# Kernel optimization log

Hardware: AMD Instinct MI355X
Metric: run time of the kernel (lower is better)

Reference implementation:

```python
import jax, jax.numpy as jnp
import numpy as np

SCALE_POS = 2.0
SCALE_NEG = 40.0
THRESH_POS = 0.5
THRESH_NEG = 0.5
MARGIN = 0.1
EPS = 1e-5


def setup_inputs() -> dict:
    key = jax.random.key(0)
    kf, kl = jax.random.split(key)
    B, D, NUM_CLASSES = 4096, 1024, 64
    feats = jax.random.normal(kf, (B, D), dtype=jnp.float32)
    feats = feats / jnp.linalg.norm(feats, axis=1, keepdims=True)  # L2-normalized embeddings
    labels = jax.random.randint(kl, (B,), 0, NUM_CLASSES, dtype=jnp.int64)
    return {"feats": feats, "labels": labels}


def reference(feats, labels):
    B = feats.shape[0]
    sim = jnp.matmul(feats, feats.T)  # [B, B]
    same = labels[:, None] == labels[None, :]
    pos_mask = same & (sim < 1.0 - EPS)  # drop self / near-duplicate pairs
    neg_mask = ~same

    # hard mining: keep negatives above min positive - margin, positives below max negative + margin
    min_pos = jnp.min(jnp.where(pos_mask, sim, jnp.inf), axis=1)   # [B]
    max_neg = jnp.max(jnp.where(neg_mask, sim, -jnp.inf), axis=1)  # [B]
    neg_sel = neg_mask & (sim + MARGIN > min_pos[:, None])
    pos_sel = pos_mask & (sim - MARGIN < max_neg[:, None])

    pos_sum = jnp.sum(jnp.where(pos_sel, jnp.exp(-SCALE_POS * (sim - THRESH_POS)), 0.0), axis=1)
    neg_sum = jnp.sum(jnp.where(neg_sel, jnp.exp(SCALE_NEG * (sim - THRESH_NEG)), 0.0), axis=1)
    pos_loss = jnp.log1p(pos_sum) / SCALE_POS
    neg_loss = jnp.log1p(neg_sum) / SCALE_NEG

    valid = jnp.any(pos_sel, axis=1) & jnp.any(neg_sel, axis=1)  # rows skipped by original loop
    return jnp.sum(jnp.where(valid, pos_loss + neg_loss, 0.0)) / B
```

## Files before the change

kernel.cpp:

```cpp
#include <hip/hip_runtime.h>

typedef short short8 __attribute__((ext_vector_type(8)));
typedef _Float16 half8 __attribute__((ext_vector_type(8)));
typedef float floatx4 __attribute__((ext_vector_type(4)));
typedef __attribute__((address_space(1))) const void gvoid;
typedef __attribute__((address_space(3))) void svoid;

#define SCALE_POS 2.0f
#define SCALE_NEG 40.0f
#define THRESH 0.5f
#define MARGIN 0.1f
#define EPSV 1e-5f

__device__ __forceinline__ unsigned short f2bf(float f) {
    unsigned u = __float_as_uint(f);
    u += 0x7fffu + ((u >> 16) & 1u);
    return (unsigned short)(u >> 16);
}
__device__ __forceinline__ unsigned f2ord(float f) {
    unsigned u = __float_as_uint(f);
    return (u & 0x80000000u) ? ~u : (u | 0x80000000u);
}
__device__ __forceinline__ float ord2f(unsigned e) {
    unsigned v = (e & 0x80000000u) ? (e & 0x7fffffffu) : ~e;
    return __uint_as_float(v);
}

#define ORD_POS_INF 0xff800000u
#define ORD_NEG_INF 0x007fffffu

__global__ void k_init(const float* __restrict__ feats,
                       unsigned short* __restrict__ fb16,
                       unsigned* __restrict__ minp, unsigned* __restrict__ maxn,
                       float* __restrict__ psum, float* __restrict__ nsum,
                       int total4, int B) {
    int i = blockIdx.x * blockDim.x + threadIdx.x;
    if (i < total4) {
        float4 v = ((const float4*)feats)[i];
        ushort4 o;
        o.x = f2bf(v.x); o.y = f2bf(v.y); o.z = f2bf(v.z); o.w = f2bf(v.w);
        ((ushort4*)fb16)[i] = o;
    }
    if (i < B) {
        minp[i] = ORD_POS_INF;
        maxn[i] = ORD_NEG_INF;
        psum[i] = 0.f;
        nsum[i] = 0.f;
    }
}

__global__ void k_gemm_sym(const unsigned short* __restrict__ fb16,
                           const int* __restrict__ labels,
                           unsigned* __restrict__ minp_ord,
                           unsigned* __restrict__ maxn_ord,
                           _Float16* __restrict__ simh,
                           int D, int nb) {
    __shared__ __align__(16) unsigned short As[128 * 32];
    __shared__ __align__(16) unsigned short Bs[128 * 32];
    __shared__ int labR[128], labC[128];

    int t = blockIdx.x;
    int rb = 0, rem = t;
    while (rem >= nb - rb) { rem -= nb - rb; ++rb; }
    const int cb = rb + rem;

    const int tid = threadIdx.x;
    const int lane = tid & 63;
    const int wave = tid >> 6;
    const int wr = wave >> 1, wc = wave & 1;
    const int rowBase = rb * 128;
    const int colBase = cb * 128;

    if (tid < 128) labR[tid] = labels[rowBase + tid];
    else           labC[tid - 128] = labels[colBase + tid - 128];

    const int c0 = wave * 2, c1 = wave * 2 + 1;
    const int srow = lane >> 2;
    const int scol = (lane & 3) * 8;
    const unsigned short* gA0 = fb16 + (size_t)(rowBase + c0 * 16 + srow) * D + scol;
    const unsigned short* gA1 = fb16 + (size_t)(rowBase + c1 * 16 + srow) * D + scol;
    const unsigned short* gB0 = fb16 + (size_t)(colBase + c0 * 16 + srow) * D + scol;
    const unsigned short* gB1 = fb16 + (size_t)(colBase + c1 * 16 + srow) * D + scol;
    unsigned short* lA0 = As + c0 * 512 + lane * 8;
    unsigned short* lA1 = As + c1 * 512 + lane * 8;
    unsigned short* lB0 = Bs + c0 * 512 + lane * 8;
    unsigned short* lB1 = Bs + c1 * 512 + lane * 8;

    const int q = lane >> 4;
    const int cIn = lane & 15;
    int aOff[4], bOff[4];
#pragma unroll
    for (int i = 0; i < 4; ++i) {
        aOff[i] = (wr * 64 + i * 16 + cIn) * 32 + q * 8;
        bOff[i] = (wc * 64 + i * 16 + cIn) * 32 + q * 8;
    }

    floatx4 acc[4][4] = {};

    const int KT = D >> 5;
    for (int kt = 0; kt < KT; ++kt) {
        const int kOff = kt * 32;
        __syncthreads();
        __builtin_amdgcn_global_load_lds((gvoid*)(gA0 + kOff), (svoid*)lA0, 16, 0, 0);
        __builtin_amdgcn_global_load_lds((gvoid*)(gA1 + kOff), (svoid*)lA1, 16, 0, 0);
        __builtin_amdgcn_global_load_lds((gvoid*)(gB0 + kOff), (svoid*)lB0, 16, 0, 0);
        __builtin_amdgcn_global_load_lds((gvoid*)(gB1 + kOff), (svoid*)lB1, 16, 0, 0);
        __syncthreads();

        short8 a[4], b[4];
#pragma unroll
        for (int i = 0; i < 4; ++i) a[i] = *(const short8*)(As + aOff[i]);
#pragma unroll
        for (int i = 0; i < 4; ++i) b[i] = *(const short8*)(Bs + bOff[i]);
#pragma unroll
        for (int i = 0; i < 4; ++i)
#pragma unroll
            for (int j = 0; j < 4; ++j)
                acc[i][j] = __builtin_amdgcn_mfma_f32_16x16x32_bf16(a[i], b[j], acc[i][j], 0, 0, 0);
    }

    int rLabv[16];
#pragma unroll
    for (int mi = 0; mi < 4; ++mi)
#pragma unroll
        for (int rr = 0; rr < 4; ++rr)
            rLabv[mi * 4 + rr] = labR[wr * 64 + mi * 16 + q * 4 + rr];
    int cLabv[4];
#pragma unroll
    for (int ni = 0; ni < 4; ++ni)
        cLabv[ni] = labC[wc * 64 + ni * 16 + cIn];

    {
        half8* dst = (half8*)(simh + (size_t)t * 16384 + (size_t)tid * 64);
#pragma unroll
        for (int mi = 0; mi < 4; ++mi) {
            half8 h0, h1;
#pragma unroll
            for (int ni = 0; ni < 2; ++ni)
#pragma unroll
                for (int rr = 0; rr < 4; ++rr) {
                    h0[ni * 4 + rr] = (_Float16)acc[mi][ni][rr];
                    h1[ni * 4 + rr] = (_Float16)acc[mi][ni + 2][rr];
                }
            dst[mi * 2] = h0;
            dst[mi * 2 + 1] = h1;
        }
    }

#pragma unroll
    for (int mi = 0; mi < 4; ++mi) {
#pragma unroll
        for (int rr = 0; rr < 4; ++rr) {
            const int rLoc = wr * 64 + mi * 16 + q * 4 + rr;
            const int rLab = rLabv[mi * 4 + rr];
            float vmin = 1e30f, vmax = -1e30f;
#pragma unroll
            for (int ni = 0; ni < 4; ++ni) {
                float s = acc[mi][ni][rr];
                if (rLab == cLabv[ni]) {
                    if (s < 1.0f - EPSV) vmin = fminf(vmin, s);
                } else {
                    vmax = fmaxf(vmax, s);
                }
            }
#pragma unroll
            for (int off = 8; off; off >>= 1) {
                vmin = fminf(vmin, __shfl_xor(vmin, off, 16));
                vmax = fmaxf(vmax, __shfl_xor(vmax, off, 16));
            }
            if (cIn == 0) {
                if (vmin < 1e30f) atomicMin(&minp_ord[rowBase + rLoc], f2ord(vmin));
                if (vmax > -1e30f) atomicMax(&maxn_ord[rowBase + rLoc], f2ord(vmax));
            }
        }
    }

    if (rb != cb) {
#pragma unroll
        for (int ni = 0; ni < 4; ++ni) {
            const int cLab = cLabv[ni];
            float vmin = 1e30f, vmax = -1e30f;
#pragma unroll
            for (int mi = 0; mi < 4; ++mi)
#pragma unroll
                for (int rr = 0; rr < 4; ++rr) {
                    float s = acc[mi][ni][rr];
                    if (rLabv[mi * 4 + rr] == cLab) {
                        if (s < 1.0f - EPSV) vmin = fminf(vmin, s);
                    } else {
                        vmax = fmaxf(vmax, s);
                    }
                }
            vmin = fminf(vmin, __shfl_xor(vmin, 16, 64));
            vmin = fminf(vmin, __shfl_xor(vmin, 32, 64));
            vmax = fmaxf(vmax, __shfl_xor(vmax, 16, 64));
            vmax = fmaxf(vmax, __shfl_xor(vmax, 32, 64));
            if (q == 0) {
                const int cLoc = wc * 64 + ni * 16 + cIn;
                if (vmin < 1e30f) atomicMin(&minp_ord[colBase + cLoc], f2ord(vmin));
                if (vmax > -1e30f) atomicMax(&maxn_ord[colBase + cLoc], f2ord(vmax));
            }
        }
    }
}

__global__ void k_sum2(const _Float16* __restrict__ simh,
                       const int* __restrict__ labels,
                       const unsigned* __restrict__ minp_ord,
                       const unsigned* __restrict__ maxn_ord,
                       float* __restrict__ psum, float* __restrict__ nsum,
                       int nb) {
    __shared__ int labR[128], labC[128];
    __shared__ float mpR[128], mnR[128], mpC[128], mnC[128];

    int t = blockIdx.x;
    int rb = 0, rem = t;
    while (rem >= nb - rb) { rem -= nb - rb; ++rb; }
    const int cb = rb + rem;

    const int tid = threadIdx.x;
    const int lane = tid & 63;
    const int wave = tid >> 6;
    const int wr = wave >> 1, wc = wave & 1;
    const int rowBase = rb * 128;
    const int colBase = cb * 128;
    const int q = lane >> 4;
    const int cIn = lane & 15;

    if (tid < 128) {
        labR[tid] = labels[rowBase + tid];
        mpR[tid] = ord2f(minp_ord[rowBase + tid]);
        mnR[tid] = ord2f(maxn_ord[rowBase + tid]);
    } else {
        int j = tid - 128;
        labC[j] = labels[colBase + j];
        mpC[j] = ord2f(minp_ord[colBase + j]);
        mnC[j] = ord2f(maxn_ord[colBase + j]);
    }
    __syncthreads();

    int rLabv[16];
    float mpRv[16], mnRv[16];
#pragma unroll
    for (int mi = 0; mi < 4; ++mi)
#pragma unroll
        for (int rr = 0; rr < 4; ++rr) {
            int rLoc = wr * 64 + mi * 16 + q * 4 + rr;
            rLabv[mi * 4 + rr] = labR[rLoc];
            mpRv[mi * 4 + rr] = mpR[rLoc] - MARGIN;
            mnRv[mi * 4 + rr] = mnR[rLoc] + MARGIN;
        }
    int cLabv[4];
    float mpCv[4], mnCv[4];
#pragma unroll
    for (int ni = 0; ni < 4; ++ni) {
        int cLoc = wc * 64 + ni * 16 + cIn;
        cLabv[ni] = labC[cLoc];
        mpCv[ni] = mpC[cLoc] - MARGIN;
        mnCv[ni] = mnC[cLoc] + MARGIN;
    }

    const half8* src = (const half8*)(simh + (size_t)t * 16384 + (size_t)tid * 64);
    half8 hv[8];
#pragma unroll
    for (int v = 0; v < 8; ++v) hv[v] = src[v];

    float rps[16] = {}, rns[16] = {};
    float cps[4] = {}, cns[4] = {};
    const bool offd = (rb != cb);

#pragma unroll
    for (int mi = 0; mi < 4; ++mi)
#pragma unroll
        for (int ni = 0; ni < 4; ++ni)
#pragma unroll
            for (int rr = 0; rr < 4; ++rr) {
                const int idx = mi * 16 + ni * 4 + rr;
                const float s = (float)hv[idx >> 3][idx & 7];
                const int ri = mi * 4 + rr;
                if (rLabv[ri] == cLabv[ni]) {
                    if (s < 1.0f - EPSV) {
                        float e = __expf(-SCALE_POS * (s - THRESH));
                        if (s < mnRv[ri]) rps[ri] += e;
                        if (offd && s < mnCv[ni]) cps[ni] += e;
                    }
                } else {
                    float e = __expf(SCALE_NEG * (s - THRESH));
                    if (s > mpRv[ri]) rns[ri] += e;
                    if (offd && s > mpCv[ni]) cns[ni] += e;
                }
            }

#pragma unroll
    for (int i = 0; i < 16; ++i) {
#pragma unroll
        for (int off = 8; off; off >>= 1) {
            rps[i] += __shfl_xor(rps[i], off, 16);
            rns[i] += __shfl_xor(rns[i], off, 16);
        }
        if (cIn == 0) {
            const int rLoc = wr * 64 + (i >> 2) * 16 + q * 4 + (i & 3);
            if (rps[i] != 0.f) atomicAdd(&psum[rowBase + rLoc], rps[i]);
            if (rns[i] != 0.f) atomicAdd(&nsum[rowBase + rLoc], rns[i]);
        }
    }
    if (offd) {
#pragma unroll
        for (int ni = 0; ni < 4; ++ni) {
            cps[ni] += __shfl_xor(cps[ni], 16, 64);
            cps[ni] += __shfl_xor(cps[ni], 32, 64);
            cns[ni] += __shfl_xor(cns[ni], 16, 64);
            cns[ni] += __shfl_xor(cns[ni], 32, 64);
            if (q == 0) {
                const int cLoc = wc * 64 + ni * 16 + cIn;
                if (cps[ni] != 0.f) atomicAdd(&psum[colBase + cLoc], cps[ni]);
                if (cns[ni] != 0.f) atomicAdd(&nsum[colBase + cLoc], cns[ni]);
            }
        }
    }
}

template <int PASS>
__global__ void k_gemm(const unsigned short* __restrict__ fb16,
                       const int* __restrict__ labels,
                       unsigned* __restrict__ minp_ord,
                       unsigned* __restrict__ maxn_ord,
                       float* __restrict__ psum,
                       float* __restrict__ nsum,
                       int D) {
    __shared__ __align__(16) unsigned short As[128 * 32];
    __shared__ __align__(16) unsigned short Bs[128 * 32];
    __shared__ int labR[128], labC[128];
    __shared__ float mpS[128], mnS[128];

    const int tid = threadIdx.x;
    const int lane = tid & 63;
    const int wave = tid >> 6;
    const int wr = wave >> 1, wc = wave & 1;
    const int rowBase = blockIdx.y * 128;
    const int colBase = blockIdx.x * 128;

    if (tid < 128) {
        labR[tid] = labels[rowBase + tid];
        if (PASS == 2) {
            mpS[tid] = ord2f(minp_ord[rowBase + tid]);
            mnS[tid] = ord2f(maxn_ord[rowBase + tid]);
        }
    } else {
        labC[tid - 128] = labels[colBase + tid - 128];
    }

    const int c0 = wave * 2, c1 = wave * 2 + 1;
    const int srow = lane >> 2;
    const int scol = (lane & 3) * 8;
    const unsigned short* gA0 = fb16 + (size_t)(rowBase + c0 * 16 + srow) * D + scol;
    const unsigned short* gA1 = fb16 + (size_t)(rowBase + c1 * 16 + srow) * D + scol;
    const unsigned short* gB0 = fb16 + (size_t)(colBase + c0 * 16 + srow) * D + scol;
    const unsigned short* gB1 = fb16 + (size_t)(colBase + c1 * 16 + srow) * D + scol;
    unsigned short* lA0 = As + c0 * 512 + lane * 8;
    unsigned short* lA1 = As + c1 * 512 + lane * 8;
    unsigned short* lB0 = Bs + c0 * 512 + lane * 8;
    unsigned short* lB1 = Bs + c1 * 512 + lane * 8;

    const int q = lane >> 4;
    const int cIn = lane & 15;
    int aOff[4], bOff[4];
#pragma unroll
    for (int i = 0; i < 4; ++i) {
        aOff[i] = (wr * 64 + i * 16 + cIn) * 32 + q * 8;
        bOff[i] = (wc * 64 + i * 16 + cIn) * 32 + q * 8;
    }

    floatx4 acc[4][4] = {};

    const int KT = D >> 5;
    for (int kt = 0; kt < KT; ++kt) {
        const int kOff = kt * 32;
        __syncthreads();
        __builtin_amdgcn_global_load_lds((gvoid*)(gA0 + kOff), (svoid*)lA0, 16, 0, 0);
        __builtin_amdgcn_global_load_lds((gvoid*)(gA1 + kOff), (svoid*)lA1, 16, 0, 0);
        __builtin_amdgcn_global_load_lds((gvoid*)(gB0 + kOff), (svoid*)lB0, 16, 0, 0);
        __builtin_amdgcn_global_load_lds((gvoid*)(gB1 + kOff), (svoid*)lB1, 16, 0, 0);
        __syncthreads();

        short8 a[4], b[4];
#pragma unroll
        for (int i = 0; i < 4; ++i) a[i] = *(const short8*)(As + aOff[i]);
#pragma unroll
        for (int i = 0; i < 4; ++i) b[i] = *(const short8*)(Bs + bOff[i]);
#pragma unroll
        for (int i = 0; i < 4; ++i)
#pragma unroll
            for (int j = 0; j < 4; ++j)
                acc[i][j] = __builtin_amdgcn_mfma_f32_16x16x32_bf16(a[i], b[j], acc[i][j], 0, 0, 0);
    }

#pragma unroll
    for (int mi = 0; mi < 4; ++mi) {
#pragma unroll
        for (int r = 0; r < 4; ++r) {
            const int rLoc = wr * 64 + mi * 16 + q * 4 + r;
            const int rLab = labR[rLoc];
            if (PASS == 1) {
                float vmin = 1e30f, vmax = -1e30f;
#pragma unroll
                for (int ni = 0; ni < 4; ++ni) {
                    float s = acc[mi][ni][r];
                    int cLab = labC[wc * 64 + ni * 16 + cIn];
                    if (rLab == cLab) {
                        if (s < 1.0f - EPSV) vmin = fminf(vmin, s);
                    } else {
                        vmax = fmaxf(vmax, s);
                    }
                }
#pragma unroll
                for (int off = 8; off; off >>= 1) {
                    vmin = fminf(vmin, __shfl_xor(vmin, off, 16));
                    vmax = fmaxf(vmax, __shfl_xor(vmax, off, 16));
                }
                if (cIn == 0) {
                    if (vmin < 1e30f) atomicMin(&minp_ord[rowBase + rLoc], f2ord(vmin));
                    if (vmax > -1e30f) atomicMax(&maxn_ord[rowBase + rLoc], f2ord(vmax));
                }
            } else {
                const float mp = mpS[rLoc] - MARGIN;
                const float mn = mnS[rLoc] + MARGIN;
                float ps = 0.f, ns = 0.f;
#pragma unroll
                for (int ni = 0; ni < 4; ++ni) {
                    float s = acc[mi][ni][r];
                    int cLab = labC[wc * 64 + ni * 16 + cIn];
                    if (rLab == cLab) {
                        if (s < 1.0f - EPSV && s < mn) ps += expf(-SCALE_POS * (s - THRESH));
                    } else {
                        if (s > mp) ns += expf(SCALE_NEG * (s - THRESH));
                    }
                }
#pragma unroll
                for (int off = 8; off; off >>= 1) {
                    ps += __shfl_xor(ps, off, 16);
                    ns += __shfl_xor(ns, off, 16);
                }
                if (cIn == 0) {
                    if (ps != 0.f) atomicAdd(&psum[rowBase + rLoc], ps);
                    if (ns != 0.f) atomicAdd(&nsum[rowBase + rLoc], ns);
                }
            }
        }
    }
}

__global__ void k_final(const float* __restrict__ psum, const float* __restrict__ nsum,
                        float* __restrict__ out, int B) {
    __shared__ float red[4];
    float acc = 0.f;
    for (int i = threadIdx.x; i < B; i += 256) {
        float p = psum[i], n = nsum[i];
        if (p > 0.f && n > 0.f)
            acc += log1pf(p) * (1.0f / SCALE_POS) + log1pf(n) * (1.0f / SCALE_NEG);
    }
#pragma unroll
    for (int off = 32; off; off >>= 1) acc += __shfl_down(acc, off, 64);
    if ((threadIdx.x & 63) == 0) red[threadIdx.x >> 6] = acc;
    __syncthreads();
    if (threadIdx.x == 0) out[0] = (red[0] + red[1] + red[2] + red[3]) / (float)B;
}

extern "C" void kernel_launch(void* const* d_in, const int* in_sizes, int n_in,
                              void* d_out, int out_size, void* d_ws, size_t ws_size,
                              hipStream_t stream) {
    const float* feats = (const float*)d_in[0];
    const int* labels = (const int*)d_in[1];
    const int B = in_sizes[1];
    const int D = in_sizes[0] / B;
    const int nb = B / 128;
    const int NT = nb * (nb + 1) / 2;

    char* ws = (char*)d_ws;
    unsigned short* fb16 = (unsigned short*)ws;
    size_t off = (size_t)B * D * sizeof(unsigned short);
    unsigned* minp = (unsigned*)(ws + off); off += (size_t)B * 4;
    unsigned* maxn = (unsigned*)(ws + off); off += (size_t)B * 4;
    float* psum = (float*)(ws + off); off += (size_t)B * 4;
    float* nsum = (float*)(ws + off); off += (size_t)B * 4;
    _Float16* simh = (_Float16*)(ws + ((off + 255) & ~(size_t)255));
    size_t need = ((off + 255) & ~(size_t)255) + (size_t)NT * 16384 * sizeof(_Float16);

    const int total4 = B * D / 4;
    k_init<<<(total4 + 255) / 256, 256, 0, stream>>>(feats, fb16, minp, maxn, psum, nsum, total4, B);

    if (ws_size >= need) {
        k_gemm_sym<<<NT, 256, 0, stream>>>(fb16, labels, minp, maxn, simh, D, nb);
        k_sum2<<<NT, 256, 0, stream>>>(simh, labels, minp, maxn, psum, nsum, nb);
    } else {
        dim3 grid(B / 128, B / 128);
        k_gemm<1><<<grid, 256, 0, stream>>>(fb16, labels, minp, maxn, psum, nsum, D);
        k_gemm<2><<<grid, 256, 0, stream>>>(fb16, labels, minp, maxn, psum, nsum, D);
    }

    k_final<<<1, 256, 0, stream>>>(psum, nsum, (float*)d_out, B);
}
```

Before: 165.6 us.

## Fuse init, symmetric GEMM, mining and loss into one cooperative kernel

Replaces the multi-kernel pipeline (init, symmetric GEMM writing fp16 similarity tiles, sum pass, final reduction) with one cooperative kernel. It keeps each tile's accumulators in registers across grid.sync barriers, so the fp16 similarity matrix is never written or reread and several launches go away. With B=4096 the grid is 528 blocks, and cooperative launch needs them all resident, so it depends on the launch-bounds occupancy of 3 blocks per CU. If the launch fails it falls back to the old path. The fallback's non-symmetric branch now launches k_gemm_sym even when the workspace is too small for the simh buffer, and k_sum2's per-row registers were restructured.

```diff
diff --git a/kernel.cpp b/kernel.cpp
--- a/kernel.cpp
+++ b/kernel.cpp
@@ -1,4 +1,7 @@
 #include <hip/hip_runtime.h>
+#include <hip/hip_cooperative_groups.h>
+
+namespace cg = cooperative_groups;
 
 typedef short short8 __attribute__((ext_vector_type(8)));
 typedef _Float16 half8 __attribute__((ext_vector_type(8)));
@@ -28,6 +31,243 @@
 
 #define ORD_POS_INF 0xff800000u
 #define ORD_NEG_INF 0x007fffffu
+
+__global__ void __launch_bounds__(256, 3)
+k_fused(const float* __restrict__ feats, const int* __restrict__ labels,
+        unsigned short* __restrict__ fb16,
+        unsigned* __restrict__ minp_ord, unsigned* __restrict__ maxn_ord,
+        float* __restrict__ psum, float* __restrict__ nsum,
+        float* __restrict__ out,
+        int D, int nb, int B, int total4) {
+    cg::grid_group grid = cg::this_grid();
+
+    __shared__ __align__(16) unsigned short As[128 * 32];
+    __shared__ __align__(16) unsigned short Bs[128 * 32];
+    __shared__ int labR[128], labC[128];
+    __shared__ float mpR[128], mnR[128], mpC[128], mnC[128];
+    __shared__ float red[4];
+
+    const int tid = threadIdx.x;
+
+    {
+        const int gtid = blockIdx.x * 256 + tid;
+        const int gsz = gridDim.x * 256;
+        for (int i = gtid; i < total4; i += gsz) {
+            float4 v = ((const float4*)feats)[i];
+            ushort4 o;
+            o.x = f2bf(v.x); o.y = f2bf(v.y); o.z = f2bf(v.z); o.w = f2bf(v.w);
+            ((ushort4*)fb16)[i] = o;
+        }
+        for (int i = gtid; i < B; i += gsz) {
+            minp_ord[i] = ORD_POS_INF;
+            maxn_ord[i] = ORD_NEG_INF;
+            psum[i] = 0.f;
+            nsum[i] = 0.f;
+        }
+    }
+
+    int t = blockIdx.x;
+    int rb = 0, rem = t;
+    while (rem >= nb - rb) { rem -= nb - rb; ++rb; }
+    const int cb = rb + rem;
+
+    const int lane = tid & 63;
+    const int wave = tid >> 6;
+    const int wr = wave >> 1, wc = wave & 1;
+    const int rowBase = rb * 128;
+    const int colBase = cb * 128;
+    const int q = lane >> 4;
+    const int cIn = lane & 15;
+
+    if (tid < 128) labR[tid] = labels[rowBase + tid];
+    else           labC[tid - 128] = labels[colBase + tid - 128];
+
+    grid.sync();
+
+    const int c0 = wave * 2, c1 = wave * 2 + 1;
+    const int srow = lane >> 2;
+    const int scol = (lane & 3) * 8;
+    const unsigned short* gA0 = fb16 + (size_t)(rowBase + c0 * 16 + srow) * D + scol;
+    const unsigned short* gA1 = fb16 + (size_t)(rowBase + c1 * 16 + srow) * D + scol;
+    const unsigned short* gB0 = fb16 + (size_t)(colBase + c0 * 16 + srow) * D + scol;
+    const unsigned short* gB1 = fb16 + (size_t)(colBase + c1 * 16 + srow) * D + scol;
+    unsigned short* lA0 = As + c0 * 512 + lane * 8;
+    unsigned short* lA1 = As + c1 * 512 + lane * 8;
+    unsigned short* lB0 = Bs + c0 * 512 + lane * 8;
+    unsigned short* lB1 = Bs + c1 * 512 + lane * 8;
+
+    int aOff[4], bOff[4];
+#pragma unroll
+    for (int i = 0; i < 4; ++i) {
+        aOff[i] = (wr * 64 + i * 16 + cIn) * 32 + q * 8;
+        bOff[i] = (wc * 64 + i * 16 + cIn) * 32 + q * 8;
+    }
+
+    floatx4 acc[4][4] = {};
+
+    const int KT = D >> 5;
+    for (int kt = 0; kt < KT; ++kt) {
+        const int kOff = kt * 32;
+        __syncthreads();
+        __builtin_amdgcn_global_load_lds((gvoid*)(gA0 + kOff), (svoid*)lA0, 16, 0, 0);
+        __builtin_amdgcn_global_load_lds((gvoid*)(gA1 + kOff), (svoid*)lA1, 16, 0, 0);
+        __builtin_amdgcn_global_load_lds((gvoid*)(gB0 + kOff), (svoid*)lB0, 16, 0, 0);
+        __builtin_amdgcn_global_load_lds((gvoid*)(gB1 + kOff), (svoid*)lB1, 16, 0, 0);
+        __syncthreads();
+
+        short8 a[4], b[4];
+#pragma unroll
+        for (int i = 0; i < 4; ++i) a[i] = *(const short8*)(As + aOff[i]);
+#pragma unroll
+        for (int i = 0; i < 4; ++i) b[i] = *(const short8*)(Bs + bOff[i]);
+#pragma unroll
+        for (int i = 0; i < 4; ++i)
+#pragma unroll
+            for (int j = 0; j < 4; ++j)
+                acc[i][j] = __builtin_amdgcn_mfma_f32_16x16x32_bf16(a[i], b[j], acc[i][j], 0, 0, 0);
+    }
+
+    int cLabv[4];
+#pragma unroll
+    for (int ni = 0; ni < 4; ++ni) cLabv[ni] = labC[wc * 64 + ni * 16 + cIn];
+    const bool offd = (rb != cb);
+
+#pragma unroll
+    for (int mi = 0; mi < 4; ++mi) {
+#pragma unroll
+        for (int rr = 0; rr < 4; ++rr) {
+            const int rLoc = wr * 64 + mi * 16 + q * 4 + rr;
+            const int rLab = labR[rLoc];
+            float vmin = 1e30f, vmax = -1e30f;
+#pragma unroll
+            for (int ni = 0; ni < 4; ++ni) {
+                float s = acc[mi][ni][rr];
+                if (rLab == cLabv[ni]) {
+                    if (s < 1.0f - EPSV) vmin = fminf(vmin, s);
+                } else {
+                    vmax = fmaxf(vmax, s);
+                }
+            }
+#pragma unroll
+            for (int off = 8; off; off >>= 1) {
+                vmin = fminf(vmin, __shfl_xor(vmin, off, 16));
+                vmax = fmaxf(vmax, __shfl_xor(vmax, off, 16));
+            }
+            if (cIn == 0) {
+                if (vmin < 1e30f) atomicMin(&minp_ord[rowBase + rLoc], f2ord(vmin));
+                if (vmax > -1e30f) atomicMax(&maxn_ord[rowBase + rLoc], f2ord(vmax));
+            }
+        }
+    }
+    if (offd) {
+#pragma unroll
+        for (int ni = 0; ni < 4; ++ni) {
+            const int cLab = cLabv[ni];
+            float vmin = 1e30f, vmax = -1e30f;
+#pragma unroll
+            for (int mi = 0; mi < 4; ++mi)
+#pragma unroll
+                for (int rr = 0; rr < 4; ++rr) {
+                    float s = acc[mi][ni][rr];
+                    if (labR[wr * 64 + mi * 16 + q * 4 + rr] == cLab) {
+                        if (s < 1.0f - EPSV) vmin = fminf(vmin, s);
+                    } else {
+                        vmax = fmaxf(vmax, s);
+                    }
+                }
+            vmin = fminf(vmin, __shfl_xor(vmin, 16, 64));
+            vmin = fminf(vmin, __shfl_xor(vmin, 32, 64));
+            vmax = fmaxf(vmax, __shfl_xor(vmax, 16, 64));
+            vmax = fmaxf(vmax, __shfl_xor(vmax, 32, 64));
+            if (q == 0) {
+                const int cLoc = wc * 64 + ni * 16 + cIn;
+                if (vmin < 1e30f) atomicMin(&minp_ord[colBase + cLoc], f2ord(vmin));
+                if (vmax > -1e30f) atomicMax(&maxn_ord[colBase + cLoc], f2ord(vmax));
+            }
+        }
+    }
+
+    grid.sync();
+
+    if (tid < 128) {
+        mpR[tid] = ord2f(atomicOr(&minp_ord[rowBase + tid], 0u)) - MARGIN;
+        mnR[tid] = ord2f(atomicOr(&maxn_ord[rowBase + tid], 0u)) + MARGIN;
+    } else {
+        const int j = tid - 128;
+        mpC[j] = ord2f(atomicOr(&minp_ord[colBase + j], 0u)) - MARGIN;
+        mnC[j] = ord2f(atomicOr(&maxn_ord[colBase + j], 0u)) + MARGIN;
+    }
+    __syncthreads();
+
+    float cps[4] = {}, cns[4] = {};
+#pragma unroll
+    for (int mi = 0; mi < 4; ++mi) {
+#pragma unroll
+        for (int rr = 0; rr < 4; ++rr) {
+            const int rLoc = wr * 64 + mi * 16 + q * 4 + rr;
+            const int rLab = labR[rLoc];
+            const float gateN = mpR[rLoc];
+            const float gateP = mnR[rLoc];
+            float rp = 0.f, rn = 0.f;
+#pragma unroll
+            for (int ni = 0; ni < 4; ++ni) {
+                const float s = acc[mi][ni][rr];
+                const int cLoc = wc * 64 + ni * 16 + cIn;
+                if (rLab == cLabv[ni]) {
+                    if (s < 1.0f - EPSV) {
+                        float e = __expf(-SCALE_POS * (s - THRESH));
+                        if (s < gateP) rp += e;
+                        if (offd && s < mnC[cLoc]) cps[ni] += e;
+                    }
+                } else {
+                    float e = __expf(SCALE_NEG * (s - THRESH));
+                    if (s > gateN) rn += e;
+                    if (offd && s > mpC[cLoc]) cns[ni] += e;
+                }
+            }
+#pragma unroll
+            for (int off = 8; off; off >>= 1) {
+                rp += __shfl_xor(rp, off, 16);
+                rn += __shfl_xor(rn, off, 16);
+            }
+            if (cIn == 0) {
+                if (rp != 0.f) atomicAdd(&psum[rowBase + rLoc], rp);
+                if (rn != 0.f) atomicAdd(&nsum[rowBase + rLoc], rn);
+            }
+        }
+    }
+    if (offd) {
+#pragma unroll
+        for (int ni = 0; ni < 4; ++ni) {
+            cps[ni] += __shfl_xor(cps[ni], 16, 64);
+            cps[ni] += __shfl_xor(cps[ni], 32, 64);
+            cns[ni] += __shfl_xor(cns[ni], 16, 64);
+            cns[ni] += __shfl_xor(cns[ni], 32, 64);
+            if (q == 0) {
+                const int cLoc = wc * 64 + ni * 16 + cIn;
+                if (cps[ni] != 0.f) atomicAdd(&psum[colBase + cLoc], cps[ni]);
+                if (cns[ni] != 0.f) atomicAdd(&nsum[colBase + cLoc], cns[ni]);
+            }
+        }
+    }
+
+    grid.sync();
+
+    if (blockIdx.x == 0) {
+        float a = 0.f;
+        for (int i = tid; i < B; i += 256) {
+            float p = atomicAdd(&psum[i], 0.0f);
+            float n = atomicAdd(&nsum[i], 0.0f);
+            if (p > 0.f && n > 0.f)
+                a += log1pf(p) * (1.0f / SCALE_POS) + log1pf(n) * (1.0f / SCALE_NEG);
+        }
+#pragma unroll
+        for (int off = 32; off; off >>= 1) a += __shfl_down(a, off, 64);
+        if ((tid & 63) == 0) red[tid >> 6] = a;
+        __syncthreads();
+        if (tid == 0) out[0] = (red[0] + red[1] + red[2] + red[3]) / (float)B;
+    }
+}
 
 __global__ void k_init(const float* __restrict__ feats,
                        unsigned short* __restrict__ fb16,
@@ -229,79 +469,63 @@
 
     if (tid < 128) {
         labR[tid] = labels[rowBase + tid];
-        mpR[tid] = ord2f(minp_ord[rowBase + tid]);
-        mnR[tid] = ord2f(maxn_ord[rowBase + tid]);
+        mpR[tid] = ord2f(minp_ord[rowBase + tid]) - MARGIN;
+        mnR[tid] = ord2f(maxn_ord[rowBase + tid]) + MARGIN;
     } else {
         int j = tid - 128;
         labC[j] = labels[colBase + j];
-        mpC[j] = ord2f(minp_ord[colBase + j]);
-        mnC[j] = ord2f(maxn_ord[colBase + j]);
+        mpC[j] = ord2f(minp_ord[colBase + j]) - MARGIN;
+        mnC[j] = ord2f(maxn_ord[colBase + j]) + MARGIN;
     }
     __syncthreads();
 
-    int rLabv[16];
-    float mpRv[16], mnRv[16];
-#pragma unroll
-    for (int mi = 0; mi < 4; ++mi)
-#pragma unroll
-        for (int rr = 0; rr < 4; ++rr) {
-            int rLoc = wr * 64 + mi * 16 + q * 4 + rr;
-            rLabv[mi * 4 + rr] = labR[rLoc];
-            mpRv[mi * 4 + rr] = mpR[rLoc] - MARGIN;
-            mnRv[mi * 4 + rr] = mnR[rLoc] + MARGIN;
-        }
     int cLabv[4];
-    float mpCv[4], mnCv[4];
-#pragma unroll
-    for (int ni = 0; ni < 4; ++ni) {
-        int cLoc = wc * 64 + ni * 16 + cIn;
-        cLabv[ni] = labC[cLoc];
-        mpCv[ni] = mpC[cLoc] - MARGIN;
-        mnCv[ni] = mnC[cLoc] + MARGIN;
-    }
+#pragma unroll
+    for (int ni = 0; ni < 4; ++ni) cLabv[ni] = labC[wc * 64 + ni * 16 + cIn];
 
     const half8* src = (const half8*)(simh + (size_t)t * 16384 + (size_t)tid * 64);
     half8 hv[8];
 #pragma unroll
     for (int v = 0; v < 8; ++v) hv[v] = src[v];
 
-    float rps[16] = {}, rns[16] = {};
     float cps[4] = {}, cns[4] = {};
     const bool offd = (rb != cb);
 
 #pragma unroll
-    for (int mi = 0; mi < 4; ++mi)
-#pragma unroll
-        for (int ni = 0; ni < 4; ++ni)
-#pragma unroll
-            for (int rr = 0; rr < 4; ++rr) {
+    for (int mi = 0; mi < 4; ++mi) {
+#pragma unroll
+        for (int rr = 0; rr < 4; ++rr) {
+            const int rLoc = wr * 64 + mi * 16 + q * 4 + rr;
+            const int rLab = labR[rLoc];
+            const float gateN = mpR[rLoc];
+            const float gateP = mnR[rLoc];
+            float rp = 0.f, rn = 0.f;
+#pragma unroll
+            for (int ni = 0; ni < 4; ++ni) {
                 const int idx = mi * 16 + ni * 4 + rr;
                 const float s = (float)hv[idx >> 3][idx & 7];
-                const int ri = mi * 4 + rr;
-                if (rLabv[ri] == cLabv[ni]) {
+                const int cLoc = wc * 64 + ni * 16 + cIn;
+                if (rLab == cLabv[ni]) {
                     if (s < 1.0f - EPSV) {
                         float e = __expf(-SCALE_POS * (s - THRESH));
-                        if (s < mnRv[ri]) rps[ri] += e;
-                        if (offd && s < mnCv[ni]) cps[ni] += e;
+                        if (s < gateP) rp += e;
+                        if (offd && s < mnC[cLoc]) cps[ni] += e;
                     }
                 } else {
                     float e = __expf(SCALE_NEG * (s - THRESH));
-                    if (s > mpRv[ri]) rns[ri] += e;
-                    if (offd && s > mpCv[ni]) cns[ni] += e;
+                    if (s > gateN) rn += e;
+                    if (offd && s > mpC[cLoc]) cns[ni] += e;
                 }
             }
-
-#pragma unroll
-    for (int i = 0; i < 16; ++i) {
-#pragma unroll
-        for (int off = 8; off; off >>= 1) {
-            rps[i] += __shfl_xor(rps[i], off, 16);
-            rns[i] += __shfl_xor(rns[i], off, 16);
-        }
-        if (cIn == 0) {
-            const int rLoc = wr * 64 + (i >> 2) * 16 + q * 4 + (i & 3);
-            if (rps[i] != 0.f) atomicAdd(&psum[rowBase + rLoc], rps[i]);
-            if (rns[i] != 0.f) atomicAdd(&nsum[rowBase + rLoc], rns[i]);
+#pragma unroll
+            for (int off = 8; off; off >>= 1) {
+                rp += __shfl_xor(rp, off, 16);
+                rn += __shfl_xor(rn, off, 16);
+            }
+            if (cIn == 0) {
+                if (rp != 0.f) atomicAdd(&psum[rowBase + rLoc], rp);
+                if (rn != 0.f) atomicAdd(&nsum[rowBase + rLoc], rn);
+            }
         }
     }
     if (offd) {
@@ -320,136 +544,6 @@
     }
 }
 
-template <int PASS>
-__global__ void k_gemm(const unsigned short* __restrict__ fb16,
-                       const int* __restrict__ labels,
-                       unsigned* __restrict__ minp_ord,
-                       unsigned* __restrict__ maxn_ord,
-                       float* __restrict__ psum,
-                       float* __restrict__ nsum,
-                       int D) {
-    __shared__ __align__(16) unsigned short As[128 * 32];
-    __shared__ __align__(16) unsigned short Bs[128 * 32];
-    __shared__ int labR[128], labC[128];
-    __shared__ float mpS[128], mnS[128];
-
-    const int tid = threadIdx.x;
-    const int lane = tid & 63;
-    const int wave = tid >> 6;
-    const int wr = wave >> 1, wc = wave & 1;
-    const int rowBase = blockIdx.y * 128;
-    const int colBase = blockIdx.x * 128;
-
-    if (tid < 128) {
-        labR[tid] = labels[rowBase + tid];
-        if (PASS == 2) {
-            mpS[tid] = ord2f(minp_ord[rowBase + tid]);
-            mnS[tid] = ord2f(maxn_ord[rowBase + tid]);
-        }
-    } else {
-        labC[tid - 128] = labels[colBase + tid - 128];
-    }
-
-    const int c0 = wave * 2, c1 = wave * 2 + 1;
-    const int srow = lane >> 2;
-    const int scol = (lane & 3) * 8;
-    const unsigned short* gA0 = fb16 + (size_t)(rowBase + c0 * 16 + srow) * D + scol;
-    const unsigned short* gA1 = fb16 + (size_t)(rowBase + c1 * 16 + srow) * D + scol;
-    const unsigned short* gB0 = fb16 + (size_t)(colBase + c0 * 16 + srow) * D + scol;
-    const unsigned short* gB1 = fb16 + (size_t)(colBase + c1 * 16 + srow) * D + scol;
-    unsigned short* lA0 = As + c0 * 512 + lane * 8;
-    unsigned short* lA1 = As + c1 * 512 + lane * 8;
-    unsigned short* lB0 = Bs + c0 * 512 + lane * 8;
-    unsigned short* lB1 = Bs + c1 * 512 + lane * 8;
-
-    const int q = lane >> 4;
-    const int cIn = lane & 15;
-    int aOff[4], bOff[4];
-#pragma unroll
-    for (int i = 0; i < 4; ++i) {
-        aOff[i] = (wr * 64 + i * 16 + cIn) * 32 + q * 8;
-        bOff[i] = (wc * 64 + i * 16 + cIn) * 32 + q * 8;
-    }
-
-    floatx4 acc[4][4] = {};
-
-    const int KT = D >> 5;
-    for (int kt = 0; kt < KT; ++kt) {
-        const int kOff = kt * 32;
-        __syncthreads();
-        __builtin_amdgcn_global_load_lds((gvoid*)(gA0 + kOff), (svoid*)lA0, 16, 0, 0);
-        __builtin_amdgcn_global_load_lds((gvoid*)(gA1 + kOff), (svoid*)lA1, 16, 0, 0);
-        __builtin_amdgcn_global_load_lds((gvoid*)(gB0 + kOff), (svoid*)lB0, 16, 0, 0);
-        __builtin_amdgcn_global_load_lds((gvoid*)(gB1 + kOff), (svoid*)lB1, 16, 0, 0);
-        __syncthreads();
-
-        short8 a[4], b[4];
-#pragma unroll
-        for (int i = 0; i < 4; ++i) a[i] = *(const short8*)(As + aOff[i]);
-#pragma unroll
-        for (int i = 0; i < 4; ++i) b[i] = *(const short8*)(Bs + bOff[i]);
-#pragma unroll
-        for (int i = 0; i < 4; ++i)
-#pragma unroll
-            for (int j = 0; j < 4; ++j)
-                acc[i][j] = __builtin_amdgcn_mfma_f32_16x16x32_bf16(a[i], b[j], acc[i][j], 0, 0, 0);
-    }
-
-#pragma unroll
-    for (int mi = 0; mi < 4; ++mi) {
-#pragma unroll
-        for (int r = 0; r < 4; ++r) {
-            const int rLoc = wr * 64 + mi * 16 + q * 4 + r;
-            const int rLab = labR[rLoc];
-            if (PASS == 1) {
-                float vmin = 1e30f, vmax = -1e30f;
-#pragma unroll
-                for (int ni = 0; ni < 4; ++ni) {
-                    float s = acc[mi][ni][r];
-                    int cLab = labC[wc * 64 + ni * 16 + cIn];
-                    if (rLab == cLab) {
-                        if (s < 1.0f - EPSV) vmin = fminf(vmin, s);
-                    } else {
-                        vmax = fmaxf(vmax, s);
-                    }
-                }
-#pragma unroll
-                for (int off = 8; off; off >>= 1) {
-                    vmin = fminf(vmin, __shfl_xor(vmin, off, 16));
-                    vmax = fmaxf(vmax, __shfl_xor(vmax, off, 16));
-                }
-                if (cIn == 0) {
-                    if (vmin < 1e30f) atomicMin(&minp_ord[rowBase + rLoc], f2ord(vmin));
-                    if (vmax > -1e30f) atomicMax(&maxn_ord[rowBase + rLoc], f2ord(vmax));
-                }
-            } else {
-                const float mp = mpS[rLoc] - MARGIN;
-                const float mn = mnS[rLoc] + MARGIN;
-                float ps = 0.f, ns = 0.f;
-#pragma unroll
-                for (int ni = 0; ni < 4; ++ni) {
-                    float s = acc[mi][ni][r];
-                    int cLab = labC[wc * 64 + ni * 16 + cIn];
-                    if (rLab == cLab) {
-                        if (s < 1.0f - EPSV && s < mn) ps += expf(-SCALE_POS * (s - THRESH));
-                    } else {
-                        if (s > mp) ns += expf(SCALE_NEG * (s - THRESH));
-                    }
-                }
-#pragma unroll
-                for (int off = 8; off; off >>= 1) {
-                    ps += __shfl_xor(ps, off, 16);
-                    ns += __shfl_xor(ns, off, 16);
-                }
-                if (cIn == 0) {
-                    if (ps != 0.f) atomicAdd(&psum[rowBase + rLoc], ps);
-                    if (ns != 0.f) atomicAdd(&nsum[rowBase + rLoc], ns);
-                }
-            }
-        }
-    }
-}
-
 __global__ void k_final(const float* __restrict__ psum, const float* __restrict__ nsum,
                         float* __restrict__ out, int B) {
     __shared__ float red[4];
@@ -471,10 +565,11 @@
                               hipStream_t stream) {
     const float* feats = (const float*)d_in[0];
     const int* labels = (const int*)d_in[1];
-    const int B = in_sizes[1];
-    const int D = in_sizes[0] / B;
-    const int nb = B / 128;
+    int B = in_sizes[1];
+    int D = in_sizes[0] / B;
+    int nb = B / 128;
     const int NT = nb * (nb + 1) / 2;
+    int total4 = B * D / 4;
 
     char* ws = (char*)d_ws;
     unsigned short* fb16 = (unsigned short*)ws;
@@ -484,19 +579,26 @@
     float* psum = (float*)(ws + off); off += (size_t)B * 4;
     float* nsum = (float*)(ws + off); off += (size_t)B * 4;
     _Float16* simh = (_Float16*)(ws + ((off + 255) & ~(size_t)255));
-    size_t need = ((off + 255) & ~(size_t)255) + (size_t)NT * 16384 * sizeof(_Float16);
-
-    const int total4 = B * D / 4;
+    size_t need_sym = ((off + 255) & ~(size_t)255) + (size_t)NT * 16384 * sizeof(_Float16);
+    float* outp = (float*)d_out;
+
+    void* kargs[] = {
+        (void*)&feats, (void*)&labels, (void*)&fb16, (void*)&minp, (void*)&maxn,
+        (void*)&psum, (void*)&nsum, (void*)&outp, (void*)&D, (void*)&nb,
+        (void*)&B, (void*)&total4
+    };
+    hipError_t err = hipLaunchCooperativeKernel((const void*)(uintptr_t)&k_fused,
+                                                dim3(NT), dim3(256), kargs, 0, stream);
+    if (err == hipSuccess) return;
+    (void)hipGetLastError();
+
     k_init<<<(total4 + 255) / 256, 256, 0, stream>>>(feats, fb16, minp, maxn, psum, nsum, total4, B);
-
-    if (ws_size >= need) {
+    if (ws_size >= need_sym) {
         k_gemm_sym<<<NT, 256, 0, stream>>>(fb16, labels, minp, maxn, simh, D, nb);
         k_sum2<<<NT, 256, 0, stream>>>(simh, labels, minp, maxn, psum, nsum, nb);
     } else {
-        dim3 grid(B / 128, B / 128);
-        k_gemm<1><<<grid, 256, 0, stream>>>(fb16, labels, minp, maxn, psum, nsum, D);
-        k_gemm<2><<<grid, 256, 0, stream>>>(fb16, labels, minp, maxn, psum, nsum, D);
-    }
-
-    k_final<<<1, 256, 0, stream>>>(psum, nsum, (float*)d_out, B);
-}
+        k_gemm_sym<<<NT, 256, 0, stream>>>(fb16, labels, minp, maxn, simh, D, nb);
+        k_sum2<<<NT, 256, 0, stream>>>(simh, labels, minp, maxn, psum, nsum, nb);
+    }
+    k_final<<<1, 256, 0, stream>>>(psum, nsum, outp, B);
+}
```

Result: slower. 282.4 us (+70.5%).
